# Optimization experiments

Hardware: AMD Instinct MI355X
Metric: run time of the kernel (lower is better)

The kernel has to match this reference:

```python
import jax, jax.numpy as jnp
import numpy as np

S = 4096          # state_size
H = 1024          # hidden_size (mamba d_model)
T = 32            # action_time_dim_size = action_dims[1]
ADIMS = (8, 32, 64)
ASIZE = int(np.prod(ADIMS))
NLAYERS = 4
D_INNER = 2 * H                     # expand=2
D_STATE = 128
D_CONV = 4
HEADDIM = 64
NHEADS = D_INNER // HEADDIM         # 32
CONV_DIM = D_INNER + 2 * D_STATE    # x, B, C go through the conv
D_IN_PROJ = 2 * D_INNER + 2 * D_STATE + NHEADS


def setup_inputs() -> dict:
    key = jax.random.key(0)
    ks = jax.random.split(key, 20)
    r = lambda k, shp: jax.random.normal(k, shp, dtype=jnp.float32) * 0.02
    inp = {
        "x": jax.random.normal(ks[0], (S,), dtype=jnp.float32),
        # mlp_in: Linear(S,H) -> act -> Linear(H, T*H)
        "w1": r(ks[1], (H, S)), "b1": jnp.zeros((H,), jnp.float32),
        "w2": r(ks[2], (T * H, H)), "b2": jnp.zeros((T * H,), jnp.float32),
        # 4 stacked Mamba2 layers (leading layer dim)
        "m_Win": r(ks[3], (NLAYERS, D_IN_PROJ, H)),
        "m_convw": r(ks[4], (NLAYERS, CONV_DIM, D_CONV)),
        "m_convb": jnp.zeros((NLAYERS, CONV_DIM), jnp.float32),
        "m_dtbias": jax.random.normal(ks[5], (NLAYERS, NHEADS), dtype=jnp.float32) * 0.1,
        "m_Alog": jnp.log(jax.random.uniform(ks[6], (NLAYERS, NHEADS), jnp.float32, 1.0, 16.0)),
        "m_D": jnp.ones((NLAYERS, NHEADS), jnp.float32),
        "m_normw": jnp.ones((NLAYERS, D_INNER), jnp.float32),
        "m_Wout": r(ks[7], (NLAYERS, H, D_INNER)),
        # mlp_out: Linear(T*H, H) -> act -> Linear(H, ASIZE)
        "w3": r(ks[8], (H, T * H)), "b3": jnp.zeros((H,), jnp.float32),
        "w4": r(ks[9], (ASIZE, H)), "b4": jnp.zeros((ASIZE,), jnp.float32),
    }
    return inp


def _mamba2_layer(u, p):
    # u: [T, H]. Faithful to mamba_ssm Mamba2 (ngroups=1, no biases on projections).
    zxbcdt = u @ p["Win"].T                      # [T, D_IN_PROJ]
    z = zxbcdt[:, :D_INNER]                       # gate
    xBC = zxbcdt[:, D_INNER:D_INNER + CONV_DIM]
    dt = zxbcdt[:, -NHEADS:]
    # causal depthwise conv1d (kernel D_CONV) + SiLU
    xp = jnp.pad(xBC, ((D_CONV - 1, 0), (0, 0)))
    conv = sum(xp[k:k + T] * p["convw"][:, k] for k in range(D_CONV))
    xBC = jax.nn.silu(conv + p["convb"])
    xh = xBC[:, :D_INNER].reshape(T, NHEADS, HEADDIM)
    B = xBC[:, D_INNER:D_INNER + D_STATE]         # [T, N]
    C = xBC[:, D_INNER + D_STATE:]                # [T, N]
    dt = jax.nn.softplus(dt + p["dtbias"])        # [T, NH]
    A = -jnp.exp(p["Alog"])                       # [NH]
    dA = jnp.exp(dt * A)                           # [T, NH]

    def step(h, inp):
        dA_t, dt_t, x_t, B_t, C_t = inp
        # h: [NH, HEADDIM, N]
        h = h * dA_t[:, None, None] + (dt_t[:, None] * x_t)[:, :, None] * B_t[None, None, :]
        y = jnp.einsum("hpn,n->hp", h, C_t)
        return h, y

    h0 = jnp.zeros((NHEADS, HEADDIM, D_STATE), u.dtype)
    _, ys = jax.lax.scan(step, h0, (dA, dt, xh, B, C))  # ys: [T, NH, HEADDIM]
    y = ys + p["D"][:, None] * xh
    y = y.reshape(T, D_INNER)
    # gated RMSNorm: x * silu(z), then rms-normalize
    yg = y * jax.nn.silu(z)
    y = yg * jax.lax.rsqrt(jnp.mean(yg * yg, axis=-1, keepdims=True) + 1e-5) * p["normw"]
    return y @ p["Wout"].T                        # [T, H]


def reference(x, w1, b1, w2, b2, m_Win, m_convw, m_convb, m_dtbias, m_Alog, m_D,
              m_normw, m_Wout, w3, b3, w4, b4):
    h = jax.nn.relu(x @ w1.T + b1)
    seq = (h @ w2.T + b2).reshape(T, H)           # view(1, T, H) with batch 1
    layer_params = {"Win": m_Win, "convw": m_convw, "convb": m_convb,
                    "dtbias": m_dtbias, "Alog": m_Alog, "D": m_D,
                    "normw": m_normw, "Wout": m_Wout}
    seq, _ = jax.lax.scan(lambda u, p: (_mamba2_layer(u, p), None), seq, layer_params)
    flat = seq.reshape(-1)                        # Flatten
    out = jax.nn.relu(flat @ w3.T + b3) @ w4.T + b4
    return jax.nn.sigmoid(out).reshape(ADIMS)
```

## Files before the change

kernel.cpp:

```cpp
#include <hip/hip_runtime.h>
#include <math.h>

#define T_DIM 32
#define H_DIM 1024
#define D_INNER 2048
#define D_STATE 128
#define NHEADS 32
#define HEADDIM 64
#define CONV_DIM 2304
#define D_IN_PROJ 4384
#define ASIZE_ 16384

__device__ __forceinline__ float wave_sum(float v) {
#pragma unroll
    for (int off = 32; off > 0; off >>= 1) v += __shfl_xor(v, off, 64);
    return v;
}
__device__ __forceinline__ float sigf(float x) { return 1.f / (1.f + expf(-x)); }
__device__ __forceinline__ float siluf(float x) { return x / (1.f + expf(-x)); }
__device__ __forceinline__ float softplusf(float x) { return x > 20.f ? x : log1pf(expf(x)); }

template <int ACT>
__global__ void gemv_wpr(const float* __restrict__ W, const float* __restrict__ x,
                         const float* __restrict__ b, float* __restrict__ out,
                         int M, int K) {
    int wid = threadIdx.x >> 6, lane = threadIdx.x & 63;
    int row = blockIdx.x * 4 + wid;
    if (row >= M) return;
    const float* wr = W + (size_t)row * K;
    float acc = 0.f;
    for (int k = lane * 4; k < K; k += 256) {
        float4 wv = *(const float4*)(wr + k);
        float4 xv = *(const float4*)(x + k);
        acc += wv.x * xv.x + wv.y * xv.y + wv.z * xv.z + wv.w * xv.w;
    }
    acc = wave_sum(acc);
    if (lane == 0) {
        float v = acc + b[row];
        if (ACT == 1) v = fmaxf(v, 0.f);
        if (ACT == 2) v = sigf(v);
        out[row] = v;
    }
}

__global__ void gemv_bpr_relu(const float* __restrict__ W, const float* __restrict__ x,
                              const float* __restrict__ b, float* __restrict__ out, int K) {
    int row = blockIdx.x;
    const float* wr = W + (size_t)row * K;
    float acc = 0.f;
    for (int k = threadIdx.x * 4; k < K; k += 1024) {
        float4 wv = *(const float4*)(wr + k);
        float4 xv = *(const float4*)(x + k);
        acc += wv.x * xv.x + wv.y * xv.y + wv.z * xv.z + wv.w * xv.w;
    }
    acc = wave_sum(acc);
    __shared__ float ws4[4];
    int wid = threadIdx.x >> 6, lane = threadIdx.x & 63;
    if (lane == 0) ws4[wid] = acc;
    __syncthreads();
    if (threadIdx.x == 0)
        out[row] = fmaxf(ws4[0] + ws4[1] + ws4[2] + ws4[3] + b[row], 0.f);
}

#define KC_IN 128
__global__ void gemm_in_k(const float* __restrict__ W, const float* __restrict__ U,
                          float* __restrict__ out, int M) {
    const int K = H_DIM;
    __shared__ float4 Ul[T_DIM][KC_IN / 4];
    int kbase = blockIdx.y * KC_IN;
    for (int i = threadIdx.x; i < T_DIM * (KC_IN / 4); i += 256) {
        int t = i >> 5, c4 = i & 31;
        Ul[t][c4] = *(const float4*)(U + t * K + kbase + c4 * 4);
    }
    __syncthreads();
    int j = blockIdx.x * 256 + threadIdx.x;
    if (j >= M) return;
    const float* wr = W + (size_t)j * K + kbase;
    float acc[T_DIM];
#pragma unroll
    for (int t = 0; t < T_DIM; t++) acc[t] = 0.f;
#pragma unroll 8
    for (int c4 = 0; c4 < KC_IN / 4; c4++) {
        float4 wv = *(const float4*)(wr + c4 * 4);
#pragma unroll
        for (int t = 0; t < T_DIM; t++) {
            float4 uv = Ul[t][c4];
            acc[t] = fmaf(wv.x, uv.x, acc[t]);
            acc[t] = fmaf(wv.y, uv.y, acc[t]);
            acc[t] = fmaf(wv.z, uv.z, acc[t]);
            acc[t] = fmaf(wv.w, uv.w, acc[t]);
        }
    }
#pragma unroll
    for (int t = 0; t < T_DIM; t++) atomicAdd(&out[t * M + j], acc[t]);
}

#define KC_OUT 64
__global__ void gemm_out_k(const float* __restrict__ W, const float* __restrict__ yg,
                           const float* __restrict__ psum, const float* __restrict__ normw,
                           float* __restrict__ out, float* __restrict__ zx_zero) {
    const int K = D_INNER;
    __shared__ float4 Ul[T_DIM][KC_OUT / 4];
    __shared__ float scale_s[T_DIM];
    __shared__ float ps8[8][T_DIM];
    {
        int t = threadIdx.x & 31, bc = threadIdx.x >> 5;
        float s = 0.f;
        for (int bb = bc; bb < 512; bb += 8) s += psum[bb * 32 + t];
        ps8[bc][t] = s;
    }
    __syncthreads();
    if (threadIdx.x < 32) {
        float tot = 0.f;
#pragma unroll
        for (int i = 0; i < 8; i++) tot += ps8[i][threadIdx.x];
        scale_s[threadIdx.x] = 1.f / sqrtf(tot * (1.f / (float)D_INNER) + 1e-5f);
    }
    __syncthreads();
    int kbase = blockIdx.y * KC_OUT;
    for (int i = threadIdx.x; i < T_DIM * (KC_OUT / 4); i += 256) {
        int t = i >> 4, c4 = i & 15;
        int k = kbase + c4 * 4;
        float4 v = *(const float4*)(yg + t * K + k);
        float4 nw = *(const float4*)(normw + k);
        float sc = scale_s[t];
        v.x *= sc * nw.x; v.y *= sc * nw.y; v.z *= sc * nw.z; v.w *= sc * nw.w;
        Ul[t][c4] = v;
    }
    __syncthreads();
    {
        int nth = gridDim.x * gridDim.y * 256;
        int gid = (blockIdx.y * gridDim.x + blockIdx.x) * 256 + threadIdx.x;
        for (int i = gid; i < T_DIM * D_IN_PROJ; i += nth) zx_zero[i] = 0.f;
    }
    int j = blockIdx.x * 256 + threadIdx.x;
    const float* wr = W + (size_t)j * K + kbase;
    float acc[T_DIM];
#pragma unroll
    for (int t = 0; t < T_DIM; t++) acc[t] = 0.f;
#pragma unroll 8
    for (int c4 = 0; c4 < KC_OUT / 4; c4++) {
        float4 wv = *(const float4*)(wr + c4 * 4);
#pragma unroll
        for (int t = 0; t < T_DIM; t++) {
            float4 uv = Ul[t][c4];
            acc[t] = fmaf(wv.x, uv.x, acc[t]);
            acc[t] = fmaf(wv.y, uv.y, acc[t]);
            acc[t] = fmaf(wv.z, uv.z, acc[t]);
            acc[t] = fmaf(wv.w, uv.w, acc[t]);
        }
    }
#pragma unroll
    for (int t = 0; t < T_DIM; t++) atomicAdd(&out[t * H_DIM + j], acc[t]);
}

__global__ void scan_k(const float* __restrict__ zx, const float* __restrict__ convw,
                       const float* __restrict__ convb, const float* __restrict__ dtbias,
                       const float* __restrict__ Alog, const float* __restrict__ Dp,
                       float* __restrict__ yg, float* __restrict__ psum,
                       float* __restrict__ seq_zero) {
    __shared__ float BC[T_DIM][256];
    __shared__ float ps_l[T_DIM];
    int tid = threadIdx.x;
    if (tid < 64) seq_zero[blockIdx.x * 64 + tid] = 0.f;
    if (tid < T_DIM) ps_l[tid] = 0.f;
    {
        int c = 2048 + tid;
        int col = D_INNER + c;
        float w0 = convw[c * 4], w1 = convw[c * 4 + 1], w2 = convw[c * 4 + 2], w3 = convw[c * 4 + 3];
        float cb = convb[c];
        float xm3 = 0.f, xm2 = 0.f, xm1 = 0.f;
#pragma unroll
        for (int t = 0; t < T_DIM; t++) {
            float x0 = zx[t * D_IN_PROJ + col];
            float v = fmaf(xm3, w0, fmaf(xm2, w1, fmaf(xm1, w2, fmaf(x0, w3, cb))));
            BC[t][tid] = siluf(v);
            xm3 = xm2; xm2 = xm1; xm1 = x0;
        }
    }
    __syncthreads();
    int wid = tid >> 6, lane = tid & 63;
    int hp = blockIdx.x * 4 + wid;
    int head = hp >> 6;
    int t0 = lane & 31;
    float dtv, dAv, xhv;
    {
        float draw = zx[t0 * D_IN_PROJ + (D_IN_PROJ - NHEADS) + head] + dtbias[head];
        dtv = softplusf(draw);
        dAv = expf(dtv * (-expf(Alog[head])));
        int c = hp;
        float w0 = convw[c * 4], w1 = convw[c * 4 + 1], w2 = convw[c * 4 + 2], w3 = convw[c * 4 + 3];
        float a = fmaf(zx[t0 * D_IN_PROJ + 2048 + c], w3, convb[c]);
        if (t0 >= 1) a = fmaf(zx[(t0 - 1) * D_IN_PROJ + 2048 + c], w2, a);
        if (t0 >= 2) a = fmaf(zx[(t0 - 2) * D_IN_PROJ + 2048 + c], w1, a);
        if (t0 >= 3) a = fmaf(zx[(t0 - 3) * D_IN_PROJ + 2048 + c], w0, a);
        xhv = siluf(a);
    }
    float coef_r = dtv * xhv;
    float h0 = 0.f, h1 = 0.f, ykeep = 0.f;
    for (int t = 0; t < T_DIM; t++) {
        float dA_t = __shfl(dAv, t, 64);
        float cf = __shfl(coef_r, t, 64);
        float B0 = BC[t][lane], B1 = BC[t][64 + lane];
        float C0 = BC[t][128 + lane], C1 = BC[t][192 + lane];
        h0 = fmaf(h0, dA_t, cf * B0);
        h1 = fmaf(h1, dA_t, cf * B1);
        float part = wave_sum(fmaf(h0, C0, h1 * C1));
        if (lane == t) ykeep = part;
    }
    if (lane < T_DIM) {
        float y = fmaf(Dp[head], xhv, ykeep);
        float z = zx[t0 * D_IN_PROJ + hp];
        float g = y * siluf(z);
        yg[t0 * D_INNER + hp] = g;
        atomicAdd(&ps_l[t0], g * g);
    }
    __syncthreads();
    if (tid < T_DIM) psum[blockIdx.x * T_DIM + tid] = ps_l[tid];
}

extern "C" void kernel_launch(void* const* d_in, const int* in_sizes, int n_in,
                              void* d_out, int out_size, void* d_ws, size_t ws_size,
                              hipStream_t stream) {
    const float* x = (const float*)d_in[0];
    const float* w1 = (const float*)d_in[1];
    const float* b1 = (const float*)d_in[2];
    const float* w2 = (const float*)d_in[3];
    const float* b2 = (const float*)d_in[4];
    const float* mWin = (const float*)d_in[5];
    const float* mconvw = (const float*)d_in[6];
    const float* mconvb = (const float*)d_in[7];
    const float* mdtb = (const float*)d_in[8];
    const float* mAlog = (const float*)d_in[9];
    const float* mD = (const float*)d_in[10];
    const float* mnw = (const float*)d_in[11];
    const float* mWout = (const float*)d_in[12];
    const float* w3 = (const float*)d_in[13];
    const float* b3 = (const float*)d_in[14];
    const float* w4 = (const float*)d_in[15];
    const float* b4 = (const float*)d_in[16];
    float* out = (float*)d_out;

    float* ws = (float*)d_ws;
    float* zx = ws;
    float* seqA = zx + T_DIM * D_IN_PROJ;
    float* seqB = seqA + T_DIM * H_DIM;
    float* yg = seqB + T_DIM * H_DIM;
    float* ps = yg + T_DIM * D_INNER;
    float* h1 = ps + 512 * T_DIM;
    float* a3 = h1 + H_DIM;

    hipMemsetAsync(zx, 0, (size_t)T_DIM * D_IN_PROJ * sizeof(float), stream);

    gemv_wpr<1><<<256, 256, 0, stream>>>(w1, x, b1, h1, H_DIM, 4096);
    gemv_wpr<0><<<8192, 256, 0, stream>>>(w2, h1, b2, seqA, T_DIM * H_DIM, H_DIM);

    float* cur = seqA;
    float* nxt = seqB;
    for (int l = 0; l < 4; l++) {
        dim3 gi((D_IN_PROJ + 255) / 256, H_DIM / KC_IN);
        gemm_in_k<<<gi, 256, 0, stream>>>(mWin + (size_t)l * D_IN_PROJ * H_DIM, cur, zx, D_IN_PROJ);
        scan_k<<<512, 256, 0, stream>>>(zx, mconvw + l * CONV_DIM * 4, mconvb + l * CONV_DIM,
                                        mdtb + l * NHEADS, mAlog + l * NHEADS, mD + l * NHEADS,
                                        yg, ps, nxt);
        dim3 go(H_DIM / 256, D_INNER / KC_OUT);
        gemm_out_k<<<go, 256, 0, stream>>>(mWout + (size_t)l * H_DIM * D_INNER, yg, ps,
                                           mnw + l * D_INNER, nxt, zx);
        float* tmp = cur; cur = nxt; nxt = tmp;
    }
    gemv_bpr_relu<<<1024, 256, 0, stream>>>(w3, cur, b3, a3, T_DIM * H_DIM);
    gemv_wpr<2><<<4096, 256, 0, stream>>>(w4, a3, b4, out, ASIZE_, H_DIM);
}
```

Measured before the change: 717.1 us.

## Fuse whole network into one cooperative persistent kernel with split-K partial buffers

Replaces the chain of separate kernel launches and the memset with a single cooperative kernel that walks through all stages, using grid.sync between them. The atomicAdd split-K accumulation into zx and the layer output is replaced by per-slice partial buffers that the consumers sum (8 slices for the input projection, 32 for the output projection). The aim is to remove launch gaps, atomics and the zeroing pass. In exchange it adds grid-wide barriers, extra partial-sum reads in the scan and next layer, and limits parallelism to the resident block count.

Measured after the change: 1.681 ms. 134% more time.

```diff
diff --git a/kernel.cpp b/kernel.cpp
--- a/kernel.cpp
+++ b/kernel.cpp
@@ -1,15 +1,16 @@
 #include <hip/hip_runtime.h>
+#include <hip/hip_cooperative_groups.h>
 #include <math.h>
+
+namespace cg = cooperative_groups;
 
 #define T_DIM 32
 #define H_DIM 1024
 #define D_INNER 2048
-#define D_STATE 128
 #define NHEADS 32
-#define HEADDIM 64
-#define CONV_DIM 2304
-#define D_IN_PROJ 4384
-#define ASIZE_ 16384
+#define DPROJ 4384
+#define ZX_SL 140288
+#define OUT_SL 32768
 
 __device__ __forceinline__ float wave_sum(float v) {
 #pragma unroll
@@ -19,204 +20,295 @@
 __device__ __forceinline__ float sigf(float x) { return 1.f / (1.f + expf(-x)); }
 __device__ __forceinline__ float siluf(float x) { return x / (1.f + expf(-x)); }
 __device__ __forceinline__ float softplusf(float x) { return x > 20.f ? x : log1pf(expf(x)); }
-
-template <int ACT>
-__global__ void gemv_wpr(const float* __restrict__ W, const float* __restrict__ x,
-                         const float* __restrict__ b, float* __restrict__ out,
-                         int M, int K) {
-    int wid = threadIdx.x >> 6, lane = threadIdx.x & 63;
-    int row = blockIdx.x * 4 + wid;
-    if (row >= M) return;
-    const float* wr = W + (size_t)row * K;
-    float acc = 0.f;
-    for (int k = lane * 4; k < K; k += 256) {
-        float4 wv = *(const float4*)(wr + k);
-        float4 xv = *(const float4*)(x + k);
-        acc += wv.x * xv.x + wv.y * xv.y + wv.z * xv.z + wv.w * xv.w;
-    }
-    acc = wave_sum(acc);
-    if (lane == 0) {
-        float v = acc + b[row];
-        if (ACT == 1) v = fmaxf(v, 0.f);
-        if (ACT == 2) v = sigf(v);
-        out[row] = v;
-    }
+__device__ __forceinline__ float zxr(const float* __restrict__ zxp, int idx) {
+    float a = 0.f;
+#pragma unroll
+    for (int s = 0; s < 8; s++) a += zxp[s * ZX_SL + idx];
+    return a;
 }
 
-__global__ void gemv_bpr_relu(const float* __restrict__ W, const float* __restrict__ x,
-                              const float* __restrict__ b, float* __restrict__ out, int K) {
-    int row = blockIdx.x;
-    const float* wr = W + (size_t)row * K;
-    float acc = 0.f;
-    for (int k = threadIdx.x * 4; k < K; k += 1024) {
-        float4 wv = *(const float4*)(wr + k);
-        float4 xv = *(const float4*)(x + k);
-        acc += wv.x * xv.x + wv.y * xv.y + wv.z * xv.z + wv.w * xv.w;
-    }
-    acc = wave_sum(acc);
-    __shared__ float ws4[4];
-    int wid = threadIdx.x >> 6, lane = threadIdx.x & 63;
-    if (lane == 0) ws4[wid] = acc;
-    __syncthreads();
-    if (threadIdx.x == 0)
-        out[row] = fmaxf(ws4[0] + ws4[1] + ws4[2] + ws4[3] + b[row], 0.f);
-}
-
-#define KC_IN 128
-__global__ void gemm_in_k(const float* __restrict__ W, const float* __restrict__ U,
-                          float* __restrict__ out, int M) {
-    const int K = H_DIM;
-    __shared__ float4 Ul[T_DIM][KC_IN / 4];
-    int kbase = blockIdx.y * KC_IN;
-    for (int i = threadIdx.x; i < T_DIM * (KC_IN / 4); i += 256) {
-        int t = i >> 5, c4 = i & 31;
-        Ul[t][c4] = *(const float4*)(U + t * K + kbase + c4 * 4);
-    }
-    __syncthreads();
-    int j = blockIdx.x * 256 + threadIdx.x;
-    if (j >= M) return;
-    const float* wr = W + (size_t)j * K + kbase;
-    float acc[T_DIM];
-#pragma unroll
-    for (int t = 0; t < T_DIM; t++) acc[t] = 0.f;
+__global__ __launch_bounds__(256, 2) void mega(
+    const float* __restrict__ x,   const float* __restrict__ w1, const float* __restrict__ b1,
+    const float* __restrict__ w2,  const float* __restrict__ b2,
+    const float* __restrict__ mWin, const float* __restrict__ mconvw, const float* __restrict__ mconvb,
+    const float* __restrict__ mdtb, const float* __restrict__ mAlog, const float* __restrict__ mD,
+    const float* __restrict__ mnw,  const float* __restrict__ mWout,
+    const float* __restrict__ w3,  const float* __restrict__ b3,
+    const float* __restrict__ w4,  const float* __restrict__ b4,
+    float* __restrict__ out, float* __restrict__ ws) {
+    __shared__ __align__(16) float lds[8192 + 96];
+    cg::grid_group grid = cg::this_grid();
+    const int NBv = gridDim.x;
+    const int NW = NBv * 4;
+    const int tid = threadIdx.x;
+    const int bi = blockIdx.x;
+    const int wid = tid >> 6, lane = tid & 63;
+    const int gw = bi * 4 + wid;
+    const int gtid = bi * 256 + tid;
+
+    float* h1v  = ws;
+    float* a3v  = ws + 1024;
+    float* seqA = ws + 2048;
+    float* yg   = ws + 34816;
+    float* psum = ws + 100352;
+    float* zxp  = ws + 116736;
+    float* outp = ws + 1238528;
+
+    for (int r = gw; r < H_DIM; r += NW) {
+        const float* wr = w1 + (size_t)r * 4096;
+        float acc = 0.f;
+        for (int k = lane * 4; k < 4096; k += 256) {
+            float4 wv = *(const float4*)(wr + k);
+            float4 xv = *(const float4*)(x + k);
+            acc += wv.x * xv.x + wv.y * xv.y + wv.z * xv.z + wv.w * xv.w;
+        }
+        acc = wave_sum(acc);
+        if (lane == 0) h1v[r] = fmaxf(acc + b1[r], 0.f);
+    }
+    grid.sync();
+
+    for (int r = gw; r < 32768; r += 2 * NW) {
+        const int r2 = r + NW;
+        const bool has2 = r2 < 32768;
+        const float* wr0 = w2 + (size_t)r * H_DIM;
+        const float* wr1 = w2 + (size_t)(has2 ? r2 : r) * H_DIM;
+        float a0 = 0.f, a1 = 0.f;
+        for (int k = lane * 4; k < H_DIM; k += 256) {
+            float4 xv = *(const float4*)(h1v + k);
+            float4 v0 = *(const float4*)(wr0 + k);
+            float4 v1 = *(const float4*)(wr1 + k);
+            a0 += v0.x * xv.x + v0.y * xv.y + v0.z * xv.z + v0.w * xv.w;
+            a1 += v1.x * xv.x + v1.y * xv.y + v1.z * xv.z + v1.w * xv.w;
+        }
+        a0 = wave_sum(a0); a1 = wave_sum(a1);
+        if (lane == 0) {
+            seqA[r] = a0 + b2[r];
+            if (has2) seqA[r2] = a1 + b2[r2];
+        }
+    }
+    grid.sync();
+
+    for (int l = 0; l < 4; l++) {
+        const float* Win  = mWin  + (size_t)l * DPROJ * H_DIM;
+        const float* convw = mconvw + l * 2304 * 4;
+        const float* convb = mconvb + l * 2304;
+        const float* dtb  = mdtb  + l * NHEADS;
+        const float* Alog = mAlog + l * NHEADS;
+        const float* Dp   = mD    + l * NHEADS;
+        const float* nw   = mnw   + l * D_INNER;
+        const float* Wout = mWout + (size_t)l * H_DIM * D_INNER;
+
+        for (int vb = bi; vb < 144; vb += NBv) {
+            const int ks = vb / 18, jb = vb % 18;
+            const int kbase = ks * 128;
+            float4* Ul = (float4*)lds;
+            for (int i = tid; i < 1024; i += 256) {
+                const int t = i >> 5, c4 = i & 31;
+                float4 v;
+                if (l == 0) {
+                    v = *(const float4*)(seqA + t * H_DIM + kbase + c4 * 4);
+                } else {
+                    v = make_float4(0.f, 0.f, 0.f, 0.f);
+                    const float* op = outp + t * H_DIM + kbase + c4 * 4;
 #pragma unroll 8
-    for (int c4 = 0; c4 < KC_IN / 4; c4++) {
-        float4 wv = *(const float4*)(wr + c4 * 4);
-#pragma unroll
-        for (int t = 0; t < T_DIM; t++) {
-            float4 uv = Ul[t][c4];
-            acc[t] = fmaf(wv.x, uv.x, acc[t]);
-            acc[t] = fmaf(wv.y, uv.y, acc[t]);
-            acc[t] = fmaf(wv.z, uv.z, acc[t]);
-            acc[t] = fmaf(wv.w, uv.w, acc[t]);
-        }
-    }
-#pragma unroll
-    for (int t = 0; t < T_DIM; t++) atomicAdd(&out[t * M + j], acc[t]);
-}
-
-#define KC_OUT 64
-__global__ void gemm_out_k(const float* __restrict__ W, const float* __restrict__ yg,
-                           const float* __restrict__ psum, const float* __restrict__ normw,
-                           float* __restrict__ out, float* __restrict__ zx_zero) {
-    const int K = D_INNER;
-    __shared__ float4 Ul[T_DIM][KC_OUT / 4];
-    __shared__ float scale_s[T_DIM];
-    __shared__ float ps8[8][T_DIM];
+                    for (int s = 0; s < 32; s++) {
+                        float4 o = *(const float4*)(op + s * OUT_SL);
+                        v.x += o.x; v.y += o.y; v.z += o.z; v.w += o.w;
+                    }
+                }
+                Ul[i] = v;
+            }
+            __syncthreads();
+            const int j = jb * 256 + tid;
+            if (j < DPROJ) {
+                const float* wr = Win + (size_t)j * H_DIM + kbase;
+                float acc[32];
+#pragma unroll
+                for (int t = 0; t < 32; t++) acc[t] = 0.f;
+#pragma unroll 8
+                for (int c4 = 0; c4 < 32; c4++) {
+                    float4 wv = *(const float4*)(wr + c4 * 4);
+#pragma unroll
+                    for (int t = 0; t < 32; t++) {
+                        float4 uv = Ul[t * 32 + c4];
+                        acc[t] = fmaf(wv.x, uv.x, acc[t]);
+                        acc[t] = fmaf(wv.y, uv.y, acc[t]);
+                        acc[t] = fmaf(wv.z, uv.z, acc[t]);
+                        acc[t] = fmaf(wv.w, uv.w, acc[t]);
+                    }
+                }
+                float* zo = zxp + ks * ZX_SL + j;
+#pragma unroll
+                for (int t = 0; t < 32; t++) zo[t * DPROJ] = acc[t];
+            }
+            __syncthreads();
+        }
+        grid.sync();
+
+        {
+            float* BC = lds;
+            float* ps_l = lds + 8192;
+            {
+                const int c = 2048 + tid, col = 4096 + tid;
+                const float q0 = convw[c * 4], q1 = convw[c * 4 + 1], q2 = convw[c * 4 + 2], q3 = convw[c * 4 + 3];
+                const float cb = convb[c];
+                float xm3 = 0.f, xm2 = 0.f, xm1 = 0.f;
+                for (int t = 0; t < T_DIM; t++) {
+                    float x0 = zxr(zxp, t * DPROJ + col);
+                    float v = fmaf(xm3, q0, fmaf(xm2, q1, fmaf(xm1, q2, fmaf(x0, q3, cb))));
+                    BC[t * 256 + tid] = siluf(v);
+                    xm3 = xm2; xm2 = xm1; xm1 = x0;
+                }
+            }
+            __syncthreads();
+            for (int hpb = bi; hpb < 512; hpb += NBv) {
+                const int hp = hpb * 4 + wid;
+                const int head = hp >> 6;
+                const int t0 = lane & 31;
+                if (tid < T_DIM) ps_l[tid] = 0.f;
+                __syncthreads();
+                float dtv, dAv, xhv;
+                {
+                    float draw = zxr(zxp, t0 * DPROJ + 4352 + head) + dtb[head];
+                    dtv = softplusf(draw);
+                    dAv = expf(dtv * (-expf(Alog[head])));
+                    const int c = hp;
+                    const float q0 = convw[c * 4], q1 = convw[c * 4 + 1], q2 = convw[c * 4 + 2], q3 = convw[c * 4 + 3];
+                    float a = fmaf(zxr(zxp, t0 * DPROJ + 2048 + c), q3, convb[c]);
+                    if (t0 >= 1) a = fmaf(zxr(zxp, (t0 - 1) * DPROJ + 2048 + c), q2, a);
+                    if (t0 >= 2) a = fmaf(zxr(zxp, (t0 - 2) * DPROJ + 2048 + c), q1, a);
+                    if (t0 >= 3) a = fmaf(zxr(zxp, (t0 - 3) * DPROJ + 2048 + c), q0, a);
+                    xhv = siluf(a);
+                }
+                const float coef = dtv * xhv;
+                float h0 = 0.f, h1 = 0.f, ykeep = 0.f;
+                for (int t = 0; t < T_DIM; t++) {
+                    float dA_t = __shfl(dAv, t, 64);
+                    float cf = __shfl(coef, t, 64);
+                    float B0 = BC[t * 256 + lane], B1 = BC[t * 256 + 64 + lane];
+                    float C0 = BC[t * 256 + 128 + lane], C1 = BC[t * 256 + 192 + lane];
+                    h0 = fmaf(h0, dA_t, cf * B0);
+                    h1 = fmaf(h1, dA_t, cf * B1);
+                    float part = wave_sum(fmaf(h0, C0, h1 * C1));
+                    if (lane == t) ykeep = part;
+                }
+                if (lane < T_DIM) {
+                    float y = fmaf(Dp[head], xhv, ykeep);
+                    float z = zxr(zxp, t0 * DPROJ + hp);
+                    float g = y * siluf(z);
+                    yg[t0 * D_INNER + hp] = g;
+                    atomicAdd(&ps_l[t0], g * g);
+                }
+                __syncthreads();
+                if (tid < T_DIM) psum[hpb * T_DIM + tid] = ps_l[tid];
+            }
+        }
+        grid.sync();
+
+        {
+            float4* Ul = (float4*)lds;
+            float* scale_s = lds + 2048;
+            float* ps8 = lds + 2080;
+            {
+                const int t = tid & 31, bc = tid >> 5;
+                float s = 0.f;
+                for (int bb = bc; bb < 512; bb += 8) s += psum[bb * 32 + t];
+                ps8[bc * 32 + t] = s;
+            }
+            __syncthreads();
+            if (tid < 32) {
+                float tot = 0.f;
+#pragma unroll
+                for (int i = 0; i < 8; i++) tot += ps8[i * 32 + tid];
+                scale_s[tid] = 1.f / sqrtf(tot * (1.f / (float)D_INNER) + 1e-5f);
+            }
+            __syncthreads();
+            for (int vb = bi; vb < 128; vb += NBv) {
+                const int ks = vb >> 2, jb = vb & 3;
+                const int kbase = ks * 64;
+                for (int i = tid; i < 512; i += 256) {
+                    const int t = i >> 4, c4 = i & 15;
+                    const int k = kbase + c4 * 4;
+                    float4 v = *(const float4*)(yg + t * D_INNER + k);
+                    float4 nv = *(const float4*)(nw + k);
+                    const float sc = scale_s[t];
+                    v.x *= sc * nv.x; v.y *= sc * nv.y; v.z *= sc * nv.z; v.w *= sc * nv.w;
+                    Ul[i] = v;
+                }
+                __syncthreads();
+                const int j = jb * 256 + tid;
+                const float* wr = Wout + (size_t)j * D_INNER + kbase;
+                float acc[32];
+#pragma unroll
+                for (int t = 0; t < 32; t++) acc[t] = 0.f;
+#pragma unroll 8
+                for (int c4 = 0; c4 < 16; c4++) {
+                    float4 wv = *(const float4*)(wr + c4 * 4);
+#pragma unroll
+                    for (int t = 0; t < 32; t++) {
+                        float4 uv = Ul[t * 16 + c4];
+                        acc[t] = fmaf(wv.x, uv.x, acc[t]);
+                        acc[t] = fmaf(wv.y, uv.y, acc[t]);
+                        acc[t] = fmaf(wv.z, uv.z, acc[t]);
+                        acc[t] = fmaf(wv.w, uv.w, acc[t]);
+                    }
+                }
+                float* oo = outp + ks * OUT_SL + j;
+#pragma unroll
+                for (int t = 0; t < 32; t++) oo[t * H_DIM] = acc[t];
+                __syncthreads();
+            }
+        }
+        grid.sync();
+    }
+
+    for (int i = gtid; i < 32768; i += NBv * 256) {
+        float s = 0.f;
+#pragma unroll 8
+        for (int sl = 0; sl < 32; sl++) s += outp[sl * OUT_SL + i];
+        seqA[i] = s;
+    }
+    grid.sync();
+
     {
-        int t = threadIdx.x & 31, bc = threadIdx.x >> 5;
-        float s = 0.f;
-        for (int bb = bc; bb < 512; bb += 8) s += psum[bb * 32 + t];
-        ps8[bc][t] = s;
-    }
-    __syncthreads();
-    if (threadIdx.x < 32) {
-        float tot = 0.f;
-#pragma unroll
-        for (int i = 0; i < 8; i++) tot += ps8[i][threadIdx.x];
-        scale_s[threadIdx.x] = 1.f / sqrtf(tot * (1.f / (float)D_INNER) + 1e-5f);
-    }
-    __syncthreads();
-    int kbase = blockIdx.y * KC_OUT;
-    for (int i = threadIdx.x; i < T_DIM * (KC_OUT / 4); i += 256) {
-        int t = i >> 4, c4 = i & 15;
-        int k = kbase + c4 * 4;
-        float4 v = *(const float4*)(yg + t * K + k);
-        float4 nw = *(const float4*)(normw + k);
-        float sc = scale_s[t];
-        v.x *= sc * nw.x; v.y *= sc * nw.y; v.z *= sc * nw.z; v.w *= sc * nw.w;
-        Ul[t][c4] = v;
-    }
-    __syncthreads();
-    {
-        int nth = gridDim.x * gridDim.y * 256;
-        int gid = (blockIdx.y * gridDim.x + blockIdx.x) * 256 + threadIdx.x;
-        for (int i = gid; i < T_DIM * D_IN_PROJ; i += nth) zx_zero[i] = 0.f;
-    }
-    int j = blockIdx.x * 256 + threadIdx.x;
-    const float* wr = W + (size_t)j * K + kbase;
-    float acc[T_DIM];
-#pragma unroll
-    for (int t = 0; t < T_DIM; t++) acc[t] = 0.f;
-#pragma unroll 8
-    for (int c4 = 0; c4 < KC_OUT / 4; c4++) {
-        float4 wv = *(const float4*)(wr + c4 * 4);
-#pragma unroll
-        for (int t = 0; t < T_DIM; t++) {
-            float4 uv = Ul[t][c4];
-            acc[t] = fmaf(wv.x, uv.x, acc[t]);
-            acc[t] = fmaf(wv.y, uv.y, acc[t]);
-            acc[t] = fmaf(wv.z, uv.z, acc[t]);
-            acc[t] = fmaf(wv.w, uv.w, acc[t]);
-        }
-    }
-#pragma unroll
-    for (int t = 0; t < T_DIM; t++) atomicAdd(&out[t * H_DIM + j], acc[t]);
-}
-
-__global__ void scan_k(const float* __restrict__ zx, const float* __restrict__ convw,
-                       const float* __restrict__ convb, const float* __restrict__ dtbias,
-                       const float* __restrict__ Alog, const float* __restrict__ Dp,
-                       float* __restrict__ yg, float* __restrict__ psum,
-                       float* __restrict__ seq_zero) {
-    __shared__ float BC[T_DIM][256];
-    __shared__ float ps_l[T_DIM];
-    int tid = threadIdx.x;
-    if (tid < 64) seq_zero[blockIdx.x * 64 + tid] = 0.f;
-    if (tid < T_DIM) ps_l[tid] = 0.f;
-    {
-        int c = 2048 + tid;
-        int col = D_INNER + c;
-        float w0 = convw[c * 4], w1 = convw[c * 4 + 1], w2 = convw[c * 4 + 2], w3 = convw[c * 4 + 3];
-        float cb = convb[c];
-        float xm3 = 0.f, xm2 = 0.f, xm1 = 0.f;
-#pragma unroll
-        for (int t = 0; t < T_DIM; t++) {
-            float x0 = zx[t * D_IN_PROJ + col];
-            float v = fmaf(xm3, w0, fmaf(xm2, w1, fmaf(xm1, w2, fmaf(x0, w3, cb))));
-            BC[t][tid] = siluf(v);
-            xm3 = xm2; xm2 = xm1; xm1 = x0;
-        }
-    }
-    __syncthreads();
-    int wid = tid >> 6, lane = tid & 63;
-    int hp = blockIdx.x * 4 + wid;
-    int head = hp >> 6;
-    int t0 = lane & 31;
-    float dtv, dAv, xhv;
-    {
-        float draw = zx[t0 * D_IN_PROJ + (D_IN_PROJ - NHEADS) + head] + dtbias[head];
-        dtv = softplusf(draw);
-        dAv = expf(dtv * (-expf(Alog[head])));
-        int c = hp;
-        float w0 = convw[c * 4], w1 = convw[c * 4 + 1], w2 = convw[c * 4 + 2], w3 = convw[c * 4 + 3];
-        float a = fmaf(zx[t0 * D_IN_PROJ + 2048 + c], w3, convb[c]);
-        if (t0 >= 1) a = fmaf(zx[(t0 - 1) * D_IN_PROJ + 2048 + c], w2, a);
-        if (t0 >= 2) a = fmaf(zx[(t0 - 2) * D_IN_PROJ + 2048 + c], w1, a);
-        if (t0 >= 3) a = fmaf(zx[(t0 - 3) * D_IN_PROJ + 2048 + c], w0, a);
-        xhv = siluf(a);
-    }
-    float coef_r = dtv * xhv;
-    float h0 = 0.f, h1 = 0.f, ykeep = 0.f;
-    for (int t = 0; t < T_DIM; t++) {
-        float dA_t = __shfl(dAv, t, 64);
-        float cf = __shfl(coef_r, t, 64);
-        float B0 = BC[t][lane], B1 = BC[t][64 + lane];
-        float C0 = BC[t][128 + lane], C1 = BC[t][192 + lane];
-        h0 = fmaf(h0, dA_t, cf * B0);
-        h1 = fmaf(h1, dA_t, cf * B1);
-        float part = wave_sum(fmaf(h0, C0, h1 * C1));
-        if (lane == t) ykeep = part;
-    }
-    if (lane < T_DIM) {
-        float y = fmaf(Dp[head], xhv, ykeep);
-        float z = zx[t0 * D_IN_PROJ + hp];
-        float g = y * siluf(z);
-        yg[t0 * D_INNER + hp] = g;
-        atomicAdd(&ps_l[t0], g * g);
-    }
-    __syncthreads();
-    if (tid < T_DIM) psum[blockIdx.x * T_DIM + tid] = ps_l[tid];
+        float* ws4 = lds;
+        for (int row = bi; row < H_DIM; row += NBv) {
+            const float* wr = w3 + (size_t)row * 32768;
+            float acc = 0.f;
+#pragma unroll 4
+            for (int k = tid * 4; k < 32768; k += 1024) {
+                float4 wv = *(const float4*)(wr + k);
+                float4 xv = *(const float4*)(seqA + k);
+                acc += wv.x * xv.x + wv.y * xv.y + wv.z * xv.z + wv.w * xv.w;
+            }
+            acc = wave_sum(acc);
+            __syncthreads();
+            if (lane == 0) ws4[wid] = acc;
+            __syncthreads();
+            if (tid == 0) a3v[row] = fmaxf(ws4[0] + ws4[1] + ws4[2] + ws4[3] + b3[row], 0.f);
+        }
+    }
+    grid.sync();
+
+    for (int r = gw; r < 16384; r += 2 * NW) {
+        const int r2 = r + NW;
+        const bool has2 = r2 < 16384;
+        const float* wr0 = w4 + (size_t)r * H_DIM;
+        const float* wr1 = w4 + (size_t)(has2 ? r2 : r) * H_DIM;
+        float a0 = 0.f, a1 = 0.f;
+        for (int k = lane * 4; k < H_DIM; k += 256) {
+            float4 xv = *(const float4*)(a3v + k);
+            float4 v0 = *(const float4*)(wr0 + k);
+            float4 v1 = *(const float4*)(wr1 + k);
+            a0 += v0.x * xv.x + v0.y * xv.y + v0.z * xv.z + v0.w * xv.w;
+            a1 += v1.x * xv.x + v1.y * xv.y + v1.z * xv.z + v1.w * xv.w;
+        }
+        a0 = wave_sum(a0); a1 = wave_sum(a1);
+        if (lane == 0) {
+            out[r] = sigf(a0 + b4[r]);
+            if (has2) out[r2] = sigf(a1 + b4[r2]);
+        }
+    }
 }
 
 extern "C" void kernel_launch(void* const* d_in, const int* in_sizes, int n_in,
@@ -240,34 +332,21 @@
     const float* w4 = (const float*)d_in[15];
     const float* b4 = (const float*)d_in[16];
     float* out = (float*)d_out;
-
     float* ws = (float*)d_ws;
-    float* zx = ws;
-    float* seqA = zx + T_DIM * D_IN_PROJ;
-    float* seqB = seqA + T_DIM * H_DIM;
-    float* yg = seqB + T_DIM * H_DIM;
-    float* ps = yg + T_DIM * D_INNER;
-    float* h1 = ps + 512 * T_DIM;
-    float* a3 = h1 + H_DIM;
-
-    hipMemsetAsync(zx, 0, (size_t)T_DIM * D_IN_PROJ * sizeof(float), stream);
-
-    gemv_wpr<1><<<256, 256, 0, stream>>>(w1, x, b1, h1, H_DIM, 4096);
-    gemv_wpr<0><<<8192, 256, 0, stream>>>(w2, h1, b2, seqA, T_DIM * H_DIM, H_DIM);
-
-    float* cur = seqA;
-    float* nxt = seqB;
-    for (int l = 0; l < 4; l++) {
-        dim3 gi((D_IN_PROJ + 255) / 256, H_DIM / KC_IN);
-        gemm_in_k<<<gi, 256, 0, stream>>>(mWin + (size_t)l * D_IN_PROJ * H_DIM, cur, zx, D_IN_PROJ);
-        scan_k<<<512, 256, 0, stream>>>(zx, mconvw + l * CONV_DIM * 4, mconvb + l * CONV_DIM,
-                                        mdtb + l * NHEADS, mAlog + l * NHEADS, mD + l * NHEADS,
-                                        yg, ps, nxt);
-        dim3 go(H_DIM / 256, D_INNER / KC_OUT);
-        gemm_out_k<<<go, 256, 0, stream>>>(mWout + (size_t)l * H_DIM * D_INNER, yg, ps,
-                                           mnw + l * D_INNER, nxt, zx);
-        float* tmp = cur; cur = nxt; nxt = tmp;
-    }
-    gemv_bpr_relu<<<1024, 256, 0, stream>>>(w3, cur, b3, a3, T_DIM * H_DIM);
-    gemv_wpr<2><<<4096, 256, 0, stream>>>(w4, a3, b4, out, ASIZE_, H_DIM);
+
+    int dev = 0;
+    hipGetDevice(&dev);
+    int cu = 256;
+    if (hipDeviceGetAttribute(&cu, hipDeviceAttributeMultiprocessorCount, dev) != hipSuccess || cu < 1)
+        cu = 256;
+    int mb = 1;
+    if (hipOccupancyMaxActiveBlocksPerMultiprocessor(&mb, (const void*)mega, 256, 0) != hipSuccess || mb < 1)
+        mb = 1;
+    long nb = (long)mb * (long)cu;
+    if (nb > 1024) nb = 1024;
+    if (nb < 1) nb = 1;
+
+    void* args[] = {&x, &w1, &b1, &w2, &b2, &mWin, &mconvw, &mconvb, &mdtb, &mAlog,
+                    &mD, &mnw, &mWout, &w3, &b3, &w4, &b4, &out, &ws};
+    hipLaunchCooperativeKernel((void*)mega, dim3((unsigned)nb), dim3(256), args, 0, stream);
 }
```
